# Kernel optimization log

Hardware: AMD Instinct MI355X
Metric: run time of the kernel (lower is better)

Reference implementation:

```python
import jax, jax.numpy as jnp
import numpy as np

B, N = 1, 320  # embed_dim == seq_len == N is forced by the module's bmm shapes


def setup_inputs() -> dict:
    key = jax.random.key(0)
    k1, k2, k3, k4 = jax.random.split(key, 4)
    s = jax.random.normal(k1, (B, N, N), dtype=jnp.float32)
    futrue = jax.random.normal(k2, (B, N, N, N), dtype=jnp.float32)
    # nn.Linear(embed_dim, embed_dim) params
    lim = 1.0 / np.sqrt(N)
    W = jax.random.uniform(k3, (N, N), minval=-lim, maxval=lim, dtype=jnp.float32)
    b = jax.random.uniform(k4, (N,), minval=-lim, maxval=lim, dtype=jnp.float32)
    return {"s": s, "futrue": futrue, "W": W, "b": b}


def reference(s, futrue, W, b):
    # futrue = self.fc(futrue): Linear on last dim  [B,T,T,E]
    futP = jnp.einsum('bitj,ej->bite', futrue, W) + b
    # fc = s.transpose(1,2) @ futrue : [B,1,E,T] @ [B,T,T,E] -> [B,T,E,E]
    scores = jnp.einsum('bte,bitj->biej', s, futP)
    fc = jax.nn.softmax(scores, axis=-1)          # softmax over last dim
    # vectorized loop: t_i = fc[:, i].sum(1).unsqueeze(-2).bmm(s)
    w = fc.sum(axis=2)                            # [B, T, T] (sum over e)
    out = jnp.einsum('bij,bjk->bik', w, s)        # concat of all t_i -> [B, T, E]
    return out
```

## Files before the change

kernel.cpp:

```cpp
#include <hip/hip_runtime.h>
#include <hip/hip_bf16.h>
#include <math.h>

#define N 320
#define NN (N * N)
#define SST 324

typedef float f32x16 __attribute__((ext_vector_type(16)));
typedef short s16x8  __attribute__((ext_vector_type(8)));

#define MFMA32(a, b, c) __builtin_amdgcn_mfma_f32_32x32x16_bf16((a), (b), (c), 0, 0, 0)

union U4V { uint4 q; s16x8 v; };
union UAV { unsigned u[4]; s16x8 v; };

__device__ inline void split2p(float x0, float x1, unsigned& hi, unsigned& lo) {
    unsigned u0 = __float_as_uint(x0), u1 = __float_as_uint(x1);
    hi = __builtin_amdgcn_perm(u1, u0, 0x07060302u);
    float d0 = x0 - __uint_as_float(u0 & 0xFFFF0000u);
    float d1 = x1 - __uint_as_float(u1 & 0xFFFF0000u);
    lo = __builtin_amdgcn_perm(__float_as_uint(d1), __float_as_uint(d0), 0x07060302u);
}

__global__ __launch_bounds__(256) void prep_kernel(
    const float* __restrict__ s, const float* __restrict__ W,
    float* __restrict__ wbuf, float* __restrict__ colsum,
    uint4* __restrict__ spH, uint4* __restrict__ spL,
    uint4* __restrict__ wpH, uint4* __restrict__ wpL)
{
    const int blk = blockIdx.x;
    const int tid = threadIdx.x;

    if (blk < 100) {
        ((float4*)wbuf)[blk * 256 + tid] = make_float4(0.f, 0.f, 0.f, 0.f);
        return;
    }
    if (blk == 100) {
        for (int e = tid; e < N; e += 256) {
            float a0 = 0.f, a1 = 0.f, a2 = 0.f, a3 = 0.f;
            for (int t = 0; t < N; t += 4) {
                a0 += s[(size_t)(t + 0) * N + e];
                a1 += s[(size_t)(t + 1) * N + e];
                a2 += s[(size_t)(t + 2) * N + e];
                a3 += s[(size_t)(t + 3) * N + e];
            }
            colsum[e] = (a0 + a1) + (a2 + a3);
        }
        return;
    }
    if (blk <= 150) {
        int fb = (blk - 101) * 4 + (tid >> 6);
        int l = tid & 63;
        int et = fb / 20, ts = fb % 20;
        int e = et * 32 + (l & 31);
        int t0 = ts * 16 + (l >> 5) * 8;
        unsigned hi[4], lo[4];
#pragma unroll
        for (int d = 0; d < 4; ++d)
            split2p(s[(size_t)(t0 + 2 * d) * N + e], s[(size_t)(t0 + 2 * d + 1) * N + e],
                    hi[d], lo[d]);
        spH[fb * 64 + l] = make_uint4(hi[0], hi[1], hi[2], hi[3]);
        spL[fb * 64 + l] = make_uint4(lo[0], lo[1], lo[2], lo[3]);
        return;
    }
    {
        int fb = (blk - 151) * 4 + (tid >> 6);
        int l = tid & 63;
        int jt = fb / 20, ks = fb % 20;
        int j = jt * 32 + (l & 31);
        int k0 = ks * 16 + (l >> 5) * 8;
        const float* wr = W + (size_t)j * N + k0;
        unsigned hi[4], lo[4];
#pragma unroll
        for (int d = 0; d < 4; ++d) split2p(wr[2 * d], wr[2 * d + 1], hi[d], lo[d]);
        wpH[fb * 64 + l] = make_uint4(hi[0], hi[1], hi[2], hi[3]);
        wpL[fb * 64 + l] = make_uint4(lo[0], lo[1], lo[2], lo[3]);
    }
}

#define LOAD_A(FB, AHV, ALV, TS) do {                                          \
    const float* fp_ = fbase + (size_t)((TS) * 16) * N;                        \
    _Pragma("unroll")                                                          \
    for (int j_ = 0; j_ < 8; ++j_) FB[j_] = fp_[(size_t)j_ * N];               \
    AHV = aH[(TS) * 64]; ALV = aL[(TS) * 64];                                  \
} while (0)

#define CONS_A(FB, AHV, ALV) do {                                              \
    UAV bh_, bl_;                                                              \
    _Pragma("unroll")                                                          \
    for (int d_ = 0; d_ < 4; ++d_)                                             \
        split2p(FB[2 * d_], FB[2 * d_ + 1], bh_.u[d_], bl_.u[d_]);             \
    U4V ah_; ah_.q = AHV; U4V al_; al_.q = ALV;                                \
    accA = MFMA32(ah_.v, bh_.v, accA);                                         \
    accB = MFMA32(al_.v, bh_.v, accB);                                         \
    accB = MFMA32(ah_.v, bl_.v, accB);                                         \
} while (0)

#define LOAD_B(WHV, WLV, GAH, GAL, KS) do {                                    \
    WHV = bH[(KS) * 64]; WLV = bL[(KS) * 64];                                  \
    int c0_ = (KS) * 2 + hf;                                                   \
    int aoff_ = (c0_ * 32 + (l31 ^ (c0_ & 7))) * 8;                            \
    GAH = *(const s16x8*)&GH[aoff_];                                           \
    GAL = *(const s16x8*)&GL[aoff_];                                           \
} while (0)

#define CONS_B(WHV, WLV, GAH, GAL) do {                                        \
    U4V wh_; wh_.q = WHV; U4V wl_; wl_.q = WLV;                                \
    acc2A = MFMA32(GAH, wh_.v, acc2A);                                         \
    acc2B = MFMA32(GAL, wh_.v, acc2B);                                         \
    acc2B = MFMA32(GAH, wl_.v, acc2B);                                         \
} while (0)

__global__ __launch_bounds__(640, 4) void fused_kernel(
    const float* __restrict__ fut,
    const uint4* __restrict__ spH, const uint4* __restrict__ spL,
    const uint4* __restrict__ wpH, const uint4* __restrict__ wpL,
    const float* __restrict__ bvec, const float* __restrict__ colsum,
    float* __restrict__ w)
{
    const int bid = blockIdx.x;
    const int i   = (bid / 80) * 8 + (bid & 7);
    const int et  = (bid >> 3) % 10;
    const int tid = threadIdx.x;
    const int wid = tid >> 6;
    const int lane = tid & 63;
    const int l31 = lane & 31;
    const int hf  = lane >> 5;

    __shared__ union {
        unsigned short G[2][40 * 32 * 8];
        float S[32 * SST];
    } sm;
    __shared__ float csh[32];
    __shared__ float Mfin[32];
    __shared__ float Ifin[32];

    if (tid < 32) csh[tid] = colsum[et * 32 + tid];

    f32x16 accA, accB;
#pragma unroll
    for (int r = 0; r < 16; ++r) { accA[r] = 0.f; accB[r] = 0.f; }

    const float* fbase = fut + (size_t)i * NN + (size_t)(hf * 8) * N + wid * 32 + l31;
    const uint4* aH = spH + (size_t)(et * 20) * 64 + lane;
    const uint4* aL = spL + (size_t)(et * 20) * 64 + lane;

    float fA[8], fB[8];
    uint4 ahA, alA, ahB, alB;
    LOAD_A(fA, ahA, alA, 0);
    for (int ts = 0; ts < 20; ts += 2) {
        LOAD_A(fB, ahB, alB, ts + 1);
        CONS_A(fA, ahA, alA);
        if (ts + 2 < 20) LOAD_A(fA, ahA, alA, ts + 2);
        CONS_A(fB, ahB, alB);
    }

    {
        const int c  = wid * 4 + (l31 >> 3);
        const int jj = l31 & 7;
        const int sw = c & 7;
        unsigned short* GH = sm.G[0];
        unsigned short* GL = sm.G[1];
#pragma unroll
        for (int r = 0; r < 16; ++r) {
            int e = (r & 3) + ((r >> 2) << 3) + (hf << 2);
            float x = accA[r] + accB[r];
            unsigned u = __float_as_uint(x);
            float d = x - __uint_as_float(u & 0xFFFF0000u);
            int off = (c * 32 + (e ^ sw)) * 8 + jj;
            GH[off] = (unsigned short)(u >> 16);
            GL[off] = (unsigned short)(__float_as_uint(d) >> 16);
        }
    }
    __syncthreads();

    f32x16 acc2A, acc2B;
#pragma unroll
    for (int r = 0; r < 16; ++r) { acc2A[r] = 0.f; acc2B[r] = 0.f; }

    const uint4* bH = wpH + (size_t)(wid * 20) * 64 + lane;
    const uint4* bL = wpL + (size_t)(wid * 20) * 64 + lane;
    const unsigned short* GH = sm.G[0];
    const unsigned short* GL = sm.G[1];

    uint4 whA, wlA, whB, wlB;
    s16x8 gahA, galA, gahB, galB;
    LOAD_B(whA, wlA, gahA, galA, 0);
    for (int ks = 0; ks < 20; ks += 2) {
        LOAD_B(whB, wlB, gahB, galB, ks + 1);
        CONS_B(whA, wlA, gahA, galA);
        if (ks + 2 < 20) LOAD_B(whA, wlA, gahA, galA, ks + 2);
        CONS_B(whB, wlB, gahB, galB);
    }

    const int jcol = wid * 32 + l31;
    float bj = bvec[jcol];
    float v[16];
#pragma unroll
    for (int r = 0; r < 16; ++r) {
        int e = (r & 3) + ((r >> 2) << 3) + (hf << 2);
        v[r] = acc2A[r] + acc2B[r] + csh[e] * bj;
    }

    __syncthreads();

#pragma unroll
    for (int r = 0; r < 16; ++r) {
        int e = (r & 3) + ((r >> 2) << 3) + (hf << 2);
        sm.S[e * SST + jcol] = v[r];
    }
    __syncthreads();

    const int hw = tid >> 5;
    const int li = tid & 31;
    if (hw < 16) {
#pragma unroll
        for (int rr = 0; rr < 2; ++rr) {
            int row = 2 * hw + rr;
            float x[10];
            float m = -3.4e38f;
#pragma unroll
            for (int q = 0; q < 10; ++q) {
                x[q] = sm.S[row * SST + li + 32 * q];
                m = fmaxf(m, x[q]);
            }
#pragma unroll
            for (int off = 16; off; off >>= 1) m = fmaxf(m, __shfl_xor(m, off, 64));
            float ssum = 0.f;
#pragma unroll
            for (int q = 0; q < 10; ++q) ssum += __expf(x[q] - m);
#pragma unroll
            for (int off = 16; off; off >>= 1) ssum += __shfl_xor(ssum, off, 64);
            if (li == 0) { Mfin[row] = m; Ifin[row] = 1.0f / ssum; }
        }
    }
    __syncthreads();

    float wcol = 0.f;
#pragma unroll
    for (int r = 0; r < 16; ++r) {
        int e = (r & 3) + ((r >> 2) << 3) + (hf << 2);
        wcol += __expf(v[r] - Mfin[e]) * Ifin[e];
    }
    wcol += __shfl_xor(wcol, 32, 64);
    if (hf == 0) atomicAdd(&w[(size_t)i * N + jcol], wcol);
}

__global__ __launch_bounds__(320) void out_gemm_kernel(
    const float* __restrict__ w, const float* __restrict__ s,
    float* __restrict__ out)
{
    const int i0 = blockIdx.x * 2;
    const int k = threadIdx.x;
    const float* w0 = w + (size_t)i0 * N;
    const float* w1 = w0 + N;
    float a0 = 0.f, a1 = 0.f, b0 = 0.f, b1 = 0.f;
    for (int j = 0; j < N; j += 2) {
        float s0 = s[(size_t)j * N + k];
        float s1 = s[(size_t)(j + 1) * N + k];
        a0 += w0[j] * s0; a1 += w0[j + 1] * s1;
        b0 += w1[j] * s0; b1 += w1[j + 1] * s1;
    }
    out[(size_t)i0 * N + k] = a0 + a1;
    out[(size_t)(i0 + 1) * N + k] = b0 + b1;
}

extern "C" void kernel_launch(void* const* d_in, const int* in_sizes, int n_in,
                              void* d_out, int out_size, void* d_ws, size_t ws_size,
                              hipStream_t stream)
{
    const float* s    = (const float*)d_in[0];
    const float* fut  = (const float*)d_in[1];
    const float* W    = (const float*)d_in[2];
    const float* bvec = (const float*)d_in[3];
    float* out = (float*)d_out;

    char* base = (char*)d_ws;
    float* wbuf   = (float*)base;
    float* colsum = (float*)(base + 409600);
    uint4* spH = (uint4*)(base + 410880);
    uint4* spL = (uint4*)(base + 615680);
    uint4* wpH = (uint4*)(base + 820480);
    uint4* wpL = (uint4*)(base + 1025280);

    prep_kernel<<<dim3(201), dim3(256), 0, stream>>>(
        s, W, wbuf, colsum, spH, spL, wpH, wpL);

    fused_kernel<<<dim3(3200), dim3(640), 0, stream>>>(
        fut, spH, spL, wpH, wpL, bvec, colsum, wbuf);

    out_gemm_kernel<<<dim3(N / 2), dim3(320), 0, stream>>>(wbuf, s, out);
}
```

Before: 401.2 us.

## Pre-pack futrue into bf16 hi/lo MFMA fragments in a separate chunked kernel

```diff
diff --git a/kernel.cpp b/kernel.cpp
--- a/kernel.cpp
+++ b/kernel.cpp
@@ -5,6 +5,7 @@
 #define N 320
 #define NN (N * N)
 #define SST 324
+#define TST 324
 
 typedef float f32x16 __attribute__((ext_vector_type(16)));
 typedef short s16x8  __attribute__((ext_vector_type(8)));
@@ -12,7 +13,6 @@
 #define MFMA32(a, b, c) __builtin_amdgcn_mfma_f32_32x32x16_bf16((a), (b), (c), 0, 0, 0)
 
 union U4V { uint4 q; s16x8 v; };
-union UAV { unsigned u[4]; s16x8 v; };
 
 __device__ inline void split2p(float x0, float x1, unsigned& hi, unsigned& lo) {
     unsigned u0 = __float_as_uint(x0), u1 = __float_as_uint(x1);
@@ -78,22 +78,51 @@
     }
 }
 
-#define LOAD_A(FB, AHV, ALV, TS) do {                                          \
-    const float* fp_ = fbase + (size_t)((TS) * 16) * N;                        \
-    _Pragma("unroll")                                                          \
-    for (int j_ = 0; j_ < 8; ++j_) FB[j_] = fp_[(size_t)j_ * N];               \
-    AHV = aH[(TS) * 64]; ALV = aL[(TS) * 64];                                  \
+__global__ __launch_bounds__(256) void fpack_kernel(
+    const float* __restrict__ fut, int i0,
+    uint4* __restrict__ fpH, uint4* __restrict__ fpL)
+{
+    const int ts = blockIdx.x;
+    const int ir = blockIdx.y;
+    const int tid = threadIdx.x;
+
+    __shared__ float T[16 * TST];
+
+    const float4* f4 = (const float4*)(fut + (size_t)(i0 + ir) * NN + (size_t)(ts * 16) * N);
+#pragma unroll
+    for (int v = 0; v < 5; ++v) {
+        int f = tid + 256 * v;
+        int r = f / 80, c = f % 80;
+        *(float4*)&T[r * TST + c * 4] = f4[r * 80 + c];
+    }
+    __syncthreads();
+
+    const size_t obase = ((size_t)ir * 20 + ts) * 10 * 64;
+    for (int slot = tid; slot < 640; slot += 256) {
+        int jt = slot >> 6, l = slot & 63;
+        int j = jt * 32 + (l & 31);
+        int tb = (l >> 5) * 8;
+        unsigned hi[4], lo[4];
+#pragma unroll
+        for (int d = 0; d < 4; ++d)
+            split2p(T[(tb + 2 * d) * TST + j], T[(tb + 2 * d + 1) * TST + j],
+                    hi[d], lo[d]);
+        fpH[obase + slot] = make_uint4(hi[0], hi[1], hi[2], hi[3]);
+        fpL[obase + slot] = make_uint4(lo[0], lo[1], lo[2], lo[3]);
+    }
+}
+
+#define LOAD_A(FH, FL, AH, AL, TS) do {                                        \
+    FH = fHp[(TS) * 640]; FL = fLp[(TS) * 640];                                \
+    AH = aHp[(TS) * 64];  AL = aLp[(TS) * 64];                                 \
 } while (0)
 
-#define CONS_A(FB, AHV, ALV) do {                                              \
-    UAV bh_, bl_;                                                              \
-    _Pragma("unroll")                                                          \
-    for (int d_ = 0; d_ < 4; ++d_)                                             \
-        split2p(FB[2 * d_], FB[2 * d_ + 1], bh_.u[d_], bl_.u[d_]);             \
-    U4V ah_; ah_.q = AHV; U4V al_; al_.q = ALV;                                \
-    accA = MFMA32(ah_.v, bh_.v, accA);                                         \
-    accB = MFMA32(al_.v, bh_.v, accB);                                         \
-    accB = MFMA32(ah_.v, bl_.v, accB);                                         \
+#define CONS_A(FH, FL, AH, AL) do {                                            \
+    U4V fh_; fh_.q = FH; U4V fl_; fl_.q = FL;                                  \
+    U4V ah_; ah_.q = AH; U4V al_; al_.q = AL;                                  \
+    accA = MFMA32(ah_.v, fh_.v, accA);                                         \
+    accB = MFMA32(al_.v, fh_.v, accB);                                         \
+    accB = MFMA32(ah_.v, fl_.v, accB);                                         \
 } while (0)
 
 #define LOAD_B(WHV, WLV, GAH, GAL, KS) do {                                    \
@@ -111,16 +140,17 @@
     acc2B = MFMA32(GAH, wl_.v, acc2B);                                         \
 } while (0)
 
-__global__ __launch_bounds__(640, 4) void fused_kernel(
-    const float* __restrict__ fut,
+__global__ __launch_bounds__(640, 5) void fused_kernel(
+    const uint4* __restrict__ fpH, const uint4* __restrict__ fpL,
     const uint4* __restrict__ spH, const uint4* __restrict__ spL,
     const uint4* __restrict__ wpH, const uint4* __restrict__ wpL,
     const float* __restrict__ bvec, const float* __restrict__ colsum,
-    float* __restrict__ w)
+    float* __restrict__ w, int i0, int cn)
 {
     const int bid = blockIdx.x;
-    const int i   = (bid / 80) * 8 + (bid & 7);
-    const int et  = (bid >> 3) % 10;
+    const int i_rel = bid % cn;
+    const int et    = bid / cn;
+    const int i     = i0 + i_rel;
     const int tid = threadIdx.x;
     const int wid = tid >> 6;
     const int lane = tid & 63;
@@ -141,26 +171,26 @@
 #pragma unroll
     for (int r = 0; r < 16; ++r) { accA[r] = 0.f; accB[r] = 0.f; }
 
-    const float* fbase = fut + (size_t)i * NN + (size_t)(hf * 8) * N + wid * 32 + l31;
-    const uint4* aH = spH + (size_t)(et * 20) * 64 + lane;
-    const uint4* aL = spL + (size_t)(et * 20) * 64 + lane;
-
-    float fA[8], fB[8];
-    uint4 ahA, alA, ahB, alB;
-    LOAD_A(fA, ahA, alA, 0);
+    const uint4* fHp = fpH + (size_t)i_rel * 20 * 10 * 64 + wid * 64 + lane;
+    const uint4* fLp = fpL + (size_t)i_rel * 20 * 10 * 64 + wid * 64 + lane;
+    const uint4* aHp = spH + (size_t)(et * 20) * 64 + lane;
+    const uint4* aLp = spL + (size_t)(et * 20) * 64 + lane;
+
+    uint4 fhA, flA, ahA, alA, fhB, flB, ahB, alB;
+    LOAD_A(fhA, flA, ahA, alA, 0);
     for (int ts = 0; ts < 20; ts += 2) {
-        LOAD_A(fB, ahB, alB, ts + 1);
-        CONS_A(fA, ahA, alA);
-        if (ts + 2 < 20) LOAD_A(fA, ahA, alA, ts + 2);
-        CONS_A(fB, ahB, alB);
+        LOAD_A(fhB, flB, ahB, alB, ts + 1);
+        CONS_A(fhA, flA, ahA, alA);
+        if (ts + 2 < 20) LOAD_A(fhA, flA, ahA, alA, ts + 2);
+        CONS_A(fhB, flB, ahB, alB);
     }
 
     {
         const int c  = wid * 4 + (l31 >> 3);
         const int jj = l31 & 7;
         const int sw = c & 7;
-        unsigned short* GH = sm.G[0];
-        unsigned short* GL = sm.G[1];
+        unsigned short* GHw = sm.G[0];
+        unsigned short* GLw = sm.G[1];
 #pragma unroll
         for (int r = 0; r < 16; ++r) {
             int e = (r & 3) + ((r >> 2) << 3) + (hf << 2);
@@ -168,8 +198,8 @@
             unsigned u = __float_as_uint(x);
             float d = x - __uint_as_float(u & 0xFFFF0000u);
             int off = (c * 32 + (e ^ sw)) * 8 + jj;
-            GH[off] = (unsigned short)(u >> 16);
-            GL[off] = (unsigned short)(__float_as_uint(d) >> 16);
+            GHw[off] = (unsigned short)(u >> 16);
+            GLw[off] = (unsigned short)(__float_as_uint(d) >> 16);
         }
     }
     __syncthreads();
@@ -250,19 +280,19 @@
     const float* __restrict__ w, const float* __restrict__ s,
     float* __restrict__ out)
 {
-    const int i0 = blockIdx.x * 2;
+    const int i = blockIdx.x;
     const int k = threadIdx.x;
-    const float* w0 = w + (size_t)i0 * N;
-    const float* w1 = w0 + N;
-    float a0 = 0.f, a1 = 0.f, b0 = 0.f, b1 = 0.f;
-    for (int j = 0; j < N; j += 2) {
-        float s0 = s[(size_t)j * N + k];
-        float s1 = s[(size_t)(j + 1) * N + k];
-        a0 += w0[j] * s0; a1 += w0[j + 1] * s1;
-        b0 += w1[j] * s0; b1 += w1[j + 1] * s1;
-    }
-    out[(size_t)i0 * N + k] = a0 + a1;
-    out[(size_t)(i0 + 1) * N + k] = b0 + b1;
+    const float* wr = w + (size_t)i * N;
+    float a[8];
+#pragma unroll
+    for (int u = 0; u < 8; ++u) a[u] = 0.f;
+    for (int j = 0; j < N; j += 8) {
+#pragma unroll
+        for (int u = 0; u < 8; ++u)
+            a[u] += wr[j + u] * s[(size_t)(j + u) * N + k];
+    }
+    float r = ((a[0] + a[1]) + (a[2] + a[3])) + ((a[4] + a[5]) + (a[6] + a[7]));
+    out[(size_t)i * N + k] = r;
 }
 
 extern "C" void kernel_launch(void* const* d_in, const int* in_sizes, int n_in,
@@ -282,12 +312,25 @@
     uint4* spL = (uint4*)(base + 615680);
     uint4* wpH = (uint4*)(base + 820480);
     uint4* wpL = (uint4*)(base + 1025280);
+    const size_t reserve = 1230080;
+
+    size_t avail = (ws_size > reserve) ? (ws_size - reserve) : 0;
+    long long cw = (long long)(avail / 409600);
+    int C = (cw >= 320) ? 320 : (int)cw;
+    if (C >= 8) C &= ~7;
+    if (C < 1) C = 1;
+    uint4* fpH = (uint4*)(base + reserve);
+    uint4* fpL = fpH + (size_t)C * 20 * 10 * 64;
 
     prep_kernel<<<dim3(201), dim3(256), 0, stream>>>(
         s, W, wbuf, colsum, spH, spL, wpH, wpL);
 
-    fused_kernel<<<dim3(3200), dim3(640), 0, stream>>>(
-        fut, spH, spL, wpH, wpL, bvec, colsum, wbuf);
-
-    out_gemm_kernel<<<dim3(N / 2), dim3(320), 0, stream>>>(wbuf, s, out);
-}
+    for (int i0 = 0; i0 < N; i0 += C) {
+        int cn = (N - i0 < C) ? (N - i0) : C;
+        fpack_kernel<<<dim3(20, cn), dim3(256), 0, stream>>>(fut, i0, fpH, fpL);
+        fused_kernel<<<dim3(cn * 10), dim3(640), 0, stream>>>(
+            fpH, fpL, spH, spL, wpH, wpL, bvec, colsum, wbuf, i0, cn);
+    }
+
+    out_gemm_kernel<<<dim3(N), dim3(320), 0, stream>>>(wbuf, s, out);
+}
```

New measurement: 536.4 us. 1.34x slower.
